# Kernel optimization log

Hardware: AMD Instinct MI355X
Metric: run time of the kernel (lower is better)

The kernel has to match this reference:

```python
import jax, jax.numpy as jnp
import numpy as np

NEG_INF = -9e15  # mask value used by the original module
LEAKY_SLOPE = 0.2


def setup_inputs() -> dict:
    key = jax.random.key(0)
    k1, k2, k3, k4 = jax.random.split(key, 4)
    B, N, F_in = 4, 2048, 128
    H, head_dim = 4, 32
    h = jax.random.normal(k1, (B, N, F_in), dtype=jnp.float32)
    adj = jax.random.randint(k2, (N, N), 0, 2, dtype=jnp.int32)
    W = jax.random.normal(k3, (H, F_in, head_dim), dtype=jnp.float32)
    a = jax.random.normal(k4, (H, 2 * head_dim, 1), dtype=jnp.float32)
    return {"h": h, "adj": adj, "W": W, "a": a}


def reference(h, adj, W, a):
    # h: (B, N, F_in); adj: (N, N) int; W: (H, F_in, D); a: (H, 2D, 1)
    D = W.shape[-1]
    Wh = jnp.einsum('bnf,hfd->bhnd', h, W)          # (B, H, N, D)
    # Original builds [Wh_i || Wh_j] @ a. Split a so that
    # e_ij = Wh_i . a_src + Wh_j . a_dst  (identical math, no N^2*2D concat).
    a_src = a[:, :D, 0]                              # (H, D)
    a_dst = a[:, D:, 0]                              # (H, D)
    e_src = jnp.einsum('bhnd,hd->bhn', Wh, a_src)    # (B, H, N)
    e_dst = jnp.einsum('bhnd,hd->bhn', Wh, a_dst)    # (B, H, N)
    e = jax.nn.leaky_relu(e_src[..., :, None] + e_dst[..., None, :],
                          negative_slope=LEAKY_SLOPE)  # (B, H, N, N)
    masked = jnp.where(adj[None, None] > 0, e, NEG_INF)
    attn = jax.nn.softmax(masked, axis=-1)           # dropout: eval mode (identity)
    out = jnp.einsum('bhij,bhjd->bhid', attn, Wh)    # (B, H, N, D)
    B, H, N, _ = out.shape
    # concat heads along feature dim == transpose to (B, N, H, D) then merge
    return out.transpose(0, 2, 1, 3).reshape(B, N, H * D)
```

## Files before the change

kernel.cpp:

```cpp
#include <hip/hip_runtime.h>
#include <hip/hip_bf16.h>

typedef unsigned short u16;
using f32x4 = __attribute__((ext_vector_type(4))) float;
using short8 = __attribute__((ext_vector_type(8))) short;

constexpr int B_ = 4, N_ = 2048, FIN = 128, H_ = 4, D_ = 32;
constexpr int BH = B_ * H_;

static __device__ __forceinline__ unsigned int pk_bf16(float lo, float hi) {
  unsigned int ul = __float_as_uint(lo);
  unsigned int uh = __float_as_uint(hi);
  ul = (ul + 0x7fffu + ((ul >> 16) & 1u)) >> 16;
  uh = (uh + 0x7fffu + ((uh >> 16) & 1u)) & 0xffff0000u;
  return ul | uh;
}

constexpr int NPB = 16;

__global__ __launch_bounds__(256) void wh_kernel(
    const float* __restrict__ h, const float* __restrict__ W,
    const float* __restrict__ a, u16* __restrict__ WhT,
    float* __restrict__ es, float* __restrict__ ed) {
  __shared__ float hsh[NPB][FIN];
  __shared__ float part[NPB][H_][D_];
  const int t = threadIdx.x;
  const int fh = t >> 7, hh = (t >> 5) & 3, d = t & 31;

  float Wr[64];
#pragma unroll
  for (int ff = 0; ff < 64; ++ff)
    Wr[ff] = W[hh * (FIN * D_) + (fh * 64 + ff) * D_ + d];

  const int n0 = blockIdx.x * NPB;
  for (int idx = t; idx < NPB * FIN; idx += 256)
    hsh[idx >> 7][idx & 127] = h[(size_t)n0 * FIN + idx];
  __syncthreads();

  float accs[NPB];
#pragma unroll
  for (int r = 0; r < NPB; ++r) {
    float acc = 0.f;
    const float* hr = &hsh[r][fh * 64];
#pragma unroll
    for (int f4 = 0; f4 < 16; ++f4) {
      float4 hv = *(const float4*)(hr + f4 * 4);
      acc += hv.x * Wr[f4 * 4 + 0];
      acc += hv.y * Wr[f4 * 4 + 1];
      acc += hv.z * Wr[f4 * 4 + 2];
      acc += hv.w * Wr[f4 * 4 + 3];
    }
    accs[r] = acc;
  }
  if (fh == 0) {
#pragma unroll
    for (int r = 0; r < NPB; ++r) part[r][hh][d] = accs[r];
  }
  __syncthreads();
  if (fh == 1) {
    const int b = n0 / N_;
    const int bh = b * H_ + hh;
    const int n0r = n0 & (N_ - 1);
    const float asrc = a[hh * 2 * D_ + d];
    const float adst = a[hh * 2 * D_ + D_ + d];
    union { u16 s[16]; uint4 q[2]; } wbuf;
#pragma unroll
    for (int r = 0; r < NPB; ++r) {
      const float wh = accs[r] + part[r][hh][d];
      union { __hip_bfloat16 h; u16 u; } cv;
      cv.h = __float2bfloat16(wh);
      wbuf.s[r] = cv.u;
      float vs = wh * asrc, vd = wh * adst;
#pragma unroll
      for (int o = 16; o >= 1; o >>= 1) {
        vs += __shfl_xor(vs, o, 64);
        vd += __shfl_xor(vd, o, 64);
      }
      if (d == 0) {
        es[(size_t)bh * N_ + n0r + r] = vs;
        ed[(size_t)bh * N_ + n0r + r] = vd;
      }
    }
    u16* dst = WhT + ((size_t)(bh * 32 + d)) * N_ + n0r;
    *(uint4*)dst = wbuf.q[0];
    *(uint4*)(dst + 8) = wbuf.q[1];
  }
}

__global__ __launch_bounds__(256) void pack_kernel(
    const int* __restrict__ adj, unsigned long long* __restrict__ mask) {
  const int gid = blockIdx.x * 256 + threadIdx.x;
  const int wdx = gid >> 6;
  const int lane = threadIdx.x & 63;
  const int i = wdx >> 5;
  const int jb = (wdx & 31) << 6;
  const int v = adj[(size_t)i * N_ + jb + lane];
  const unsigned long long m = __ballot(v > 0);
  if (lane == 0) mask[wdx] = m;
}

constexpr int RMROWS = 32;

__global__ __launch_bounds__(256) void rowmax_kernel(
    const float* __restrict__ ed, const unsigned int* __restrict__ mask32,
    float* __restrict__ rowmaxed) {
  __shared__ float edL[N_];
  __shared__ unsigned int msh[RMROWS][65];
  const int bh = blockIdx.x >> 6;
  const int r0 = (blockIdx.x & 63) * RMROWS;
  const int tid = threadIdx.x, lane = tid & 63, w = tid >> 6;

  const float* edb = ed + (size_t)bh * N_;
#pragma unroll
  for (int q = 0; q < 8; ++q) edL[tid + q * 256] = edb[tid + q * 256];
  const unsigned int* mrow = mask32 + (size_t)r0 * 64;
#pragma unroll
  for (int q = 0; q < 8; ++q) {
    const int idx = tid + q * 256;
    msh[idx >> 6][idx & 63] = mrow[(idx >> 6) * 64 + (idx & 63)];
  }
  __syncthreads();

  for (int r = w; r < RMROWS; r += 4) {
    float mx = -3.0e38f;
#pragma unroll
    for (int q = 0; q < 32; ++q) {
      const unsigned int mword = msh[r][q * 2 + (lane >> 5)];
      const float v = edL[q * 64 + lane];
      mx = ((mword >> (lane & 31)) & 1u) ? fmaxf(mx, v) : mx;
    }
#pragma unroll
    for (int o = 32; o >= 1; o >>= 1) mx = fmaxf(mx, __shfl_xor(mx, o, 64));
    if (lane == 0) rowmaxed[(size_t)bh * N_ + r0 + r] = mx;
  }
}

constexpr int ROWS = 32;
constexpr int KSTEPS = 32;

__global__ __launch_bounds__(256) void attn_kernel(
    const float* __restrict__ es, const float* __restrict__ ed,
    const float* __restrict__ rowmaxed, const u16* __restrict__ WhT,
    const unsigned int* __restrict__ mask32, float* __restrict__ out) {
  __shared__ float edsh[N_];
  __shared__ unsigned char maskL[ROWS * 260];
  __shared__ u16 whL[2][2][32 * 40];
  __shared__ float redc[2][2][16][32];
  __shared__ float sumsh[2][2][16];
  __shared__ float essh[ROWS];
  __shared__ float rmsh[ROWS];

  const int bh = blockIdx.x >> 6;
  const int it = blockIdx.x & 63;
  const int i0 = it * ROWS;
  const int tid = threadIdx.x, lane = tid & 63, w = tid >> 6;
  const int tile = w & 1, jh = w >> 1;

  const float* edb = ed + (size_t)bh * N_;
  float4 e0 = *(const float4*)(edb + tid * 8);
  float4 e1 = *(const float4*)(edb + tid * 8 + 4);
  *(float4*)&edsh[tid * 8] = e0;
  *(float4*)&edsh[tid * 8 + 4] = e1;

  const unsigned int* mrow = mask32 + (size_t)i0 * 64;
#pragma unroll
  for (int q = 0; q < 8; ++q) {
    const int idx = tid + q * 256;
    const int r = idx >> 6, c = idx & 63;
    ((unsigned int*)maskL)[r * 65 + c] = mrow[r * 64 + c];
  }
  if (tid < ROWS) {
    essh[tid] = es[(size_t)bh * N_ + i0 + tid];
    rmsh[tid] = rowmaxed[(size_t)bh * N_ + i0 + tid];
  }

  const int jt = tid >> 7;
  const int sr = (tid >> 2) & 31;
  const int sc = tid & 3;
  const u16* wsrc = WhT + ((size_t)(bh * 32 + sr)) * N_ + jt * 1024 + sc * 8;
  *(uint4*)&whL[0][jt][sr * 40 + sc * 8] = *(const uint4*)wsrc;
  __syncthreads();

  const int row16 = lane & 15, kg = lane >> 4;
  const int row32 = tile * 16 + row16;
  const float esr = essh[row32];
  const float xm = esr + rmsh[row32];
  const float mxr = fmaxf(xm, 0.2f * xm);

  f32x4 c0 = {}, c1 = {};
  float sum = 0.f;
  int cur = 0;

  for (int s = 0; s < KSTEPS; ++s) {
    uint4 nx;
    const bool hasnext = (s + 1 < KSTEPS);
    if (hasnext) nx = *(const uint4*)(wsrc + (s + 1) * 32);

    const int k0 = jh * 1024 + s * 32;
    const unsigned int mb = maskL[row32 * 260 + (k0 >> 3) + kg];
    const float4 ea = *(const float4*)&edsh[k0 + kg * 8];
    const float4 eb = *(const float4*)&edsh[k0 + kg * 8 + 4];
    const float ev[8] = {ea.x, ea.y, ea.z, ea.w, eb.x, eb.y, eb.z, eb.w};
    float p[8];
#pragma unroll
    for (int j = 0; j < 8; ++j) {
      const float x = esr + ev[j];
      const float y = fmaxf(x, 0.2f * x);
      float z = fminf(y - mxr, 0.f);
      z = (mb & (1u << j)) ? z : -1e30f;
      const float pj = __expf(z);
      p[j] = pj;
      sum += pj;
    }
    union { unsigned int u[4]; short8 v8; } af;
    af.u[0] = pk_bf16(p[0], p[1]);
    af.u[1] = pk_bf16(p[2], p[3]);
    af.u[2] = pk_bf16(p[4], p[5]);
    af.u[3] = pk_bf16(p[6], p[7]);

    const short8 b0 = *(const short8*)&whL[cur][jh][row16 * 40 + kg * 8];
    const short8 b1 = *(const short8*)&whL[cur][jh][(16 + row16) * 40 + kg * 8];
    c0 = __builtin_amdgcn_mfma_f32_16x16x32_bf16(af.v8, b0, c0, 0, 0, 0);
    c1 = __builtin_amdgcn_mfma_f32_16x16x32_bf16(af.v8, b1, c1, 0, 0, 0);

    __syncthreads();
    if (hasnext) {
      *(uint4*)&whL[cur ^ 1][jt][sr * 40 + sc * 8] = nx;
      __syncthreads();
    }
    cur ^= 1;
  }

  sum += __shfl_xor(sum, 16, 64);
  sum += __shfl_xor(sum, 32, 64);
  if (lane < 16) sumsh[tile][jh][lane] = sum;
#pragma unroll
  for (int r = 0; r < 4; ++r) {
    redc[tile][jh][kg * 4 + r][row16] = c0[r];
    redc[tile][jh][kg * 4 + r][16 + row16] = c1[r];
  }
  __syncthreads();

  const int r32 = tid >> 3;
  const int c4 = (tid & 7) * 4;
  const int tl = r32 >> 4, rr = r32 & 15;
  const float inv = 1.f / fmaxf(sumsh[tl][0][rr] + sumsh[tl][1][rr], 1e-30f);
  float4 o;
  o.x = (redc[tl][0][rr][c4 + 0] + redc[tl][1][rr][c4 + 0]) * inv;
  o.y = (redc[tl][0][rr][c4 + 1] + redc[tl][1][rr][c4 + 1]) * inv;
  o.z = (redc[tl][0][rr][c4 + 2] + redc[tl][1][rr][c4 + 2]) * inv;
  o.w = (redc[tl][0][rr][c4 + 3] + redc[tl][1][rr][c4 + 3]) * inv;
  const int b = bh >> 2, hh = bh & 3;
  *(float4*)&out[((size_t)(b * N_ + i0 + r32)) * (H_ * D_) + hh * 32 + c4] = o;
}

extern "C" void kernel_launch(void* const* d_in, const int* in_sizes, int n_in,
                              void* d_out, int out_size, void* d_ws,
                              size_t ws_size, hipStream_t stream) {
  const float* h = (const float*)d_in[0];
  const int* adj = (const int*)d_in[1];
  const float* W = (const float*)d_in[2];
  const float* a = (const float*)d_in[3];
  char* ws = (char*)d_ws;
  u16* WhT = (u16*)ws;
  float* es = (float*)(ws + (2u << 20));
  float* ed = (float*)(ws + (2u << 20) + (128u << 10));
  unsigned long long* mask =
      (unsigned long long*)(ws + (2u << 20) + (256u << 10));
  float* rowmaxed = (float*)(ws + (2u << 20) + (768u << 10));
  float* out = (float*)d_out;

  wh_kernel<<<B_ * N_ / NPB, 256, 0, stream>>>(h, W, a, WhT, es, ed);
  pack_kernel<<<N_ * N_ / 256, 256, 0, stream>>>(adj, mask);
  rowmax_kernel<<<BH * (N_ / RMROWS), 256, 0, stream>>>(
      ed, (const unsigned int*)mask, rowmaxed);
  attn_kernel<<<BH * (N_ / ROWS), 256, 0, stream>>>(
      es, ed, rowmaxed, WhT, (const unsigned int*)mask, out);
}
```

Measured before the change: 145.3 us.

## Fuse masked row-max into attention kernel and enlarge Wh staging chunks

Removes the separate rowmax kernel launch by computing each block's masked row maxima of ed inside the attention kernel, reusing the ed and mask tiles already staged in shared memory. The Wh staging buffer grows from 32 to 128 columns per chunk, which cuts the number of barriers in the main loop by a factor of four. Scores are pre-scaled by log2(e) so exp2f can replace __expf. Shared memory is aliased through an arena for the reduction scratch. The cost is extra ALU work per block for the row max and higher LDS use per block.

```diff
diff --git a/kernel.cpp b/kernel.cpp
--- a/kernel.cpp
+++ b/kernel.cpp
@@ -7,6 +7,7 @@
 
 constexpr int B_ = 4, N_ = 2048, FIN = 128, H_ = 4, D_ = 32;
 constexpr int BH = B_ * H_;
+constexpr float LOG2E = 1.4426950408889634f;
 
 static __device__ __forceinline__ unsigned int pk_bf16(float lo, float hi) {
   unsigned int ul = __float_as_uint(lo);
@@ -77,8 +78,8 @@
         vd += __shfl_xor(vd, o, 64);
       }
       if (d == 0) {
-        es[(size_t)bh * N_ + n0r + r] = vs;
-        ed[(size_t)bh * N_ + n0r + r] = vd;
+        es[(size_t)bh * N_ + n0r + r] = vs * LOG2E;
+        ed[(size_t)bh * N_ + n0r + r] = vd * LOG2E;
       }
     }
     u16* dst = WhT + ((size_t)(bh * 32 + d)) * N_ + n0r;
@@ -99,86 +100,63 @@
   if (lane == 0) mask[wdx] = m;
 }
 
-constexpr int RMROWS = 32;
-
-__global__ __launch_bounds__(256) void rowmax_kernel(
-    const float* __restrict__ ed, const unsigned int* __restrict__ mask32,
-    float* __restrict__ rowmaxed) {
-  __shared__ float edL[N_];
-  __shared__ unsigned int msh[RMROWS][65];
+constexpr int ROWS = 32;
+constexpr int CH = 128;
+constexpr int CHP = 136;
+constexpr int NCHUNK = 1024 / CH;
+
+__global__ __launch_bounds__(256) void attn_kernel(
+    const float* __restrict__ es, const float* __restrict__ ed,
+    const u16* __restrict__ WhT, const unsigned int* __restrict__ mask32,
+    float* __restrict__ out) {
+  __shared__ __align__(16) char arena[16640];
+  __shared__ u16 whL[2][2][32 * CHP];
+  __shared__ float essh[ROWS], rmsh[ROWS];
+
+  float* edsh = (float*)arena;
+  unsigned int* maskw = (unsigned int*)(arena + 8192);
+  unsigned char* maskb = (unsigned char*)(arena + 8192);
+
   const int bh = blockIdx.x >> 6;
-  const int r0 = (blockIdx.x & 63) * RMROWS;
+  const int i0 = (blockIdx.x & 63) * ROWS;
   const int tid = threadIdx.x, lane = tid & 63, w = tid >> 6;
+  const int tile = w & 1, jh = w >> 1;
 
   const float* edb = ed + (size_t)bh * N_;
-#pragma unroll
-  for (int q = 0; q < 8; ++q) edL[tid + q * 256] = edb[tid + q * 256];
-  const unsigned int* mrow = mask32 + (size_t)r0 * 64;
+  *(float4*)&edsh[tid * 8] = *(const float4*)(edb + tid * 8);
+  *(float4*)&edsh[tid * 8 + 4] = *(const float4*)(edb + tid * 8 + 4);
+  const unsigned int* mrow = mask32 + (size_t)i0 * 64;
 #pragma unroll
   for (int q = 0; q < 8; ++q) {
     const int idx = tid + q * 256;
-    msh[idx >> 6][idx & 63] = mrow[(idx >> 6) * 64 + (idx & 63)];
-  }
-  __syncthreads();
-
-  for (int r = w; r < RMROWS; r += 4) {
-    float mx = -3.0e38f;
-#pragma unroll
-    for (int q = 0; q < 32; ++q) {
-      const unsigned int mword = msh[r][q * 2 + (lane >> 5)];
-      const float v = edL[q * 64 + lane];
-      mx = ((mword >> (lane & 31)) & 1u) ? fmaxf(mx, v) : mx;
-    }
-#pragma unroll
-    for (int o = 32; o >= 1; o >>= 1) mx = fmaxf(mx, __shfl_xor(mx, o, 64));
-    if (lane == 0) rowmaxed[(size_t)bh * N_ + r0 + r] = mx;
-  }
-}
-
-constexpr int ROWS = 32;
-constexpr int KSTEPS = 32;
-
-__global__ __launch_bounds__(256) void attn_kernel(
-    const float* __restrict__ es, const float* __restrict__ ed,
-    const float* __restrict__ rowmaxed, const u16* __restrict__ WhT,
-    const unsigned int* __restrict__ mask32, float* __restrict__ out) {
-  __shared__ float edsh[N_];
-  __shared__ unsigned char maskL[ROWS * 260];
-  __shared__ u16 whL[2][2][32 * 40];
-  __shared__ float redc[2][2][16][32];
-  __shared__ float sumsh[2][2][16];
-  __shared__ float essh[ROWS];
-  __shared__ float rmsh[ROWS];
-
-  const int bh = blockIdx.x >> 6;
-  const int it = blockIdx.x & 63;
-  const int i0 = it * ROWS;
-  const int tid = threadIdx.x, lane = tid & 63, w = tid >> 6;
-  const int tile = w & 1, jh = w >> 1;
-
-  const float* edb = ed + (size_t)bh * N_;
-  float4 e0 = *(const float4*)(edb + tid * 8);
-  float4 e1 = *(const float4*)(edb + tid * 8 + 4);
-  *(float4*)&edsh[tid * 8] = e0;
-  *(float4*)&edsh[tid * 8 + 4] = e1;
-
-  const unsigned int* mrow = mask32 + (size_t)i0 * 64;
-#pragma unroll
-  for (int q = 0; q < 8; ++q) {
-    const int idx = tid + q * 256;
-    const int r = idx >> 6, c = idx & 63;
-    ((unsigned int*)maskL)[r * 65 + c] = mrow[r * 64 + c];
-  }
-  if (tid < ROWS) {
-    essh[tid] = es[(size_t)bh * N_ + i0 + tid];
-    rmsh[tid] = rowmaxed[(size_t)bh * N_ + i0 + tid];
-  }
+    maskw[(idx >> 6) * 65 + (idx & 63)] = mrow[(idx >> 6) * 64 + (idx & 63)];
+  }
+  if (tid < ROWS) essh[tid] = es[(size_t)bh * N_ + i0 + tid];
 
   const int jt = tid >> 7;
   const int sr = (tid >> 2) & 31;
   const int sc = tid & 3;
   const u16* wsrc = WhT + ((size_t)(bh * 32 + sr)) * N_ + jt * 1024 + sc * 8;
-  *(uint4*)&whL[0][jt][sr * 40 + sc * 8] = *(const uint4*)wsrc;
+#pragma unroll
+  for (int q = 0; q < 4; ++q)
+    *(uint4*)&whL[0][jt][sr * CHP + sc * 8 + q * 32] =
+        *(const uint4*)(wsrc + q * 32);
+  __syncthreads();
+
+#pragma unroll
+  for (int q8 = 0; q8 < 8; ++q8) {
+    const int r = w * 8 + q8;
+    float mx = -3.0e38f;
+#pragma unroll
+    for (int q = 0; q < 32; ++q) {
+      const unsigned int mword = maskw[r * 65 + q * 2 + (lane >> 5)];
+      const float v = edsh[q * 64 + lane];
+      mx = ((mword >> (lane & 31)) & 1u) ? fmaxf(mx, v) : mx;
+    }
+#pragma unroll
+    for (int o = 32; o >= 1; o >>= 1) mx = fmaxf(mx, __shfl_xor(mx, o, 64));
+    if (lane == 0) rmsh[r] = mx;
+  }
   __syncthreads();
 
   const int row16 = lane & 15, kg = lane >> 4;
@@ -191,65 +169,79 @@
   float sum = 0.f;
   int cur = 0;
 
-  for (int s = 0; s < KSTEPS; ++s) {
-    uint4 nx;
-    const bool hasnext = (s + 1 < KSTEPS);
-    if (hasnext) nx = *(const uint4*)(wsrc + (s + 1) * 32);
-
-    const int k0 = jh * 1024 + s * 32;
-    const unsigned int mb = maskL[row32 * 260 + (k0 >> 3) + kg];
-    const float4 ea = *(const float4*)&edsh[k0 + kg * 8];
-    const float4 eb = *(const float4*)&edsh[k0 + kg * 8 + 4];
-    const float ev[8] = {ea.x, ea.y, ea.z, ea.w, eb.x, eb.y, eb.z, eb.w};
-    float p[8];
-#pragma unroll
-    for (int j = 0; j < 8; ++j) {
-      const float x = esr + ev[j];
-      const float y = fmaxf(x, 0.2f * x);
-      float z = fminf(y - mxr, 0.f);
-      z = (mb & (1u << j)) ? z : -1e30f;
-      const float pj = __expf(z);
-      p[j] = pj;
-      sum += pj;
-    }
-    union { unsigned int u[4]; short8 v8; } af;
-    af.u[0] = pk_bf16(p[0], p[1]);
-    af.u[1] = pk_bf16(p[2], p[3]);
-    af.u[2] = pk_bf16(p[4], p[5]);
-    af.u[3] = pk_bf16(p[6], p[7]);
-
-    const short8 b0 = *(const short8*)&whL[cur][jh][row16 * 40 + kg * 8];
-    const short8 b1 = *(const short8*)&whL[cur][jh][(16 + row16) * 40 + kg * 8];
-    c0 = __builtin_amdgcn_mfma_f32_16x16x32_bf16(af.v8, b0, c0, 0, 0, 0);
-    c1 = __builtin_amdgcn_mfma_f32_16x16x32_bf16(af.v8, b1, c1, 0, 0, 0);
-
+  for (int c = 0; c < NCHUNK; ++c) {
+    uint4 nx[4];
+    const bool hasnext = (c + 1 < NCHUNK);
+    if (hasnext) {
+#pragma unroll
+      for (int q = 0; q < 4; ++q)
+        nx[q] = *(const uint4*)(wsrc + (c + 1) * CH + q * 32);
+    }
+#pragma unroll
+    for (int sub = 0; sub < 4; ++sub) {
+      const int k0 = jh * 1024 + c * CH + sub * 32;
+      const unsigned int mb = maskb[row32 * 260 + (k0 >> 3) + kg];
+      const float4 ea = *(const float4*)&edsh[k0 + kg * 8];
+      const float4 eb = *(const float4*)&edsh[k0 + kg * 8 + 4];
+      const float ev[8] = {ea.x, ea.y, ea.z, ea.w, eb.x, eb.y, eb.z, eb.w};
+      float p[8];
+#pragma unroll
+      for (int j = 0; j < 8; ++j) {
+        const float x = esr + ev[j];
+        const float y = fmaxf(x, 0.2f * x);
+        float z = fminf(y - mxr, 0.f);
+        z = (mb & (1u << j)) ? z : -1e30f;
+        const float pj = exp2f(z);
+        p[j] = pj;
+        sum += pj;
+      }
+      union { unsigned int u[4]; short8 v8; } af;
+      af.u[0] = pk_bf16(p[0], p[1]);
+      af.u[1] = pk_bf16(p[2], p[3]);
+      af.u[2] = pk_bf16(p[4], p[5]);
+      af.u[3] = pk_bf16(p[6], p[7]);
+
+      const u16* bbase = &whL[cur][jh][row16 * CHP + sub * 32 + kg * 8];
+      const short8 b0 = *(const short8*)bbase;
+      const short8 b1 = *(const short8*)(bbase + 16 * CHP);
+      c0 = __builtin_amdgcn_mfma_f32_16x16x32_bf16(af.v8, b0, c0, 0, 0, 0);
+      c1 = __builtin_amdgcn_mfma_f32_16x16x32_bf16(af.v8, b1, c1, 0, 0, 0);
+    }
     __syncthreads();
     if (hasnext) {
-      *(uint4*)&whL[cur ^ 1][jt][sr * 40 + sc * 8] = nx;
-      __syncthreads();
-    }
+#pragma unroll
+      for (int q = 0; q < 4; ++q)
+        *(uint4*)&whL[cur ^ 1][jt][sr * CHP + sc * 8 + q * 32] = nx[q];
+    }
+    __syncthreads();
     cur ^= 1;
   }
 
+  float* redc = (float*)arena;
+  float* sumsh = (float*)(arena + 16384);
   sum += __shfl_xor(sum, 16, 64);
   sum += __shfl_xor(sum, 32, 64);
-  if (lane < 16) sumsh[tile][jh][lane] = sum;
+  if (lane < 16) sumsh[(tile * 2 + jh) * 16 + lane] = sum;
 #pragma unroll
   for (int r = 0; r < 4; ++r) {
-    redc[tile][jh][kg * 4 + r][row16] = c0[r];
-    redc[tile][jh][kg * 4 + r][16 + row16] = c1[r];
+    redc[(((tile * 2 + jh) * 16) + kg * 4 + r) * 32 + row16] = c0[r];
+    redc[(((tile * 2 + jh) * 16) + kg * 4 + r) * 32 + 16 + row16] = c1[r];
   }
   __syncthreads();
 
   const int r32 = tid >> 3;
   const int c4 = (tid & 7) * 4;
   const int tl = r32 >> 4, rr = r32 & 15;
-  const float inv = 1.f / fmaxf(sumsh[tl][0][rr] + sumsh[tl][1][rr], 1e-30f);
+  const float inv =
+      1.f / fmaxf(sumsh[(tl * 2 + 0) * 16 + rr] + sumsh[(tl * 2 + 1) * 16 + rr],
+                  1e-30f);
+  const float* r0 = &redc[((tl * 2 + 0) * 16 + rr) * 32 + c4];
+  const float* r1 = &redc[((tl * 2 + 1) * 16 + rr) * 32 + c4];
   float4 o;
-  o.x = (redc[tl][0][rr][c4 + 0] + redc[tl][1][rr][c4 + 0]) * inv;
-  o.y = (redc[tl][0][rr][c4 + 1] + redc[tl][1][rr][c4 + 1]) * inv;
-  o.z = (redc[tl][0][rr][c4 + 2] + redc[tl][1][rr][c4 + 2]) * inv;
-  o.w = (redc[tl][0][rr][c4 + 3] + redc[tl][1][rr][c4 + 3]) * inv;
+  o.x = (r0[0] + r1[0]) * inv;
+  o.y = (r0[1] + r1[1]) * inv;
+  o.z = (r0[2] + r1[2]) * inv;
+  o.w = (r0[3] + r1[3]) * inv;
   const int b = bh >> 2, hh = bh & 3;
   *(float4*)&out[((size_t)(b * N_ + i0 + r32)) * (H_ * D_) + hh * 32 + c4] = o;
 }
@@ -267,13 +259,10 @@
   float* ed = (float*)(ws + (2u << 20) + (128u << 10));
   unsigned long long* mask =
       (unsigned long long*)(ws + (2u << 20) + (256u << 10));
-  float* rowmaxed = (float*)(ws + (2u << 20) + (768u << 10));
   float* out = (float*)d_out;
 
   wh_kernel<<<B_ * N_ / NPB, 256, 0, stream>>>(h, W, a, WhT, es, ed);
   pack_kernel<<<N_ * N_ / 256, 256, 0, stream>>>(adj, mask);
-  rowmax_kernel<<<BH * (N_ / RMROWS), 256, 0, stream>>>(
-      ed, (const unsigned int*)mask, rowmaxed);
   attn_kernel<<<BH * (N_ / ROWS), 256, 0, stream>>>(
-      es, ed, rowmaxed, WhT, (const unsigned int*)mask, out);
-}
+      es, ed, WhT, (const unsigned int*)mask, out);
+}
```

After: 181.1 us. 24.7% more time.
